# Optimization experiments

Hardware: AMD Instinct MI355X
Metric: run time of the kernel (lower is better)

## Reference

```python
import jax, jax.numpy as jnp
import numpy as np

B, A, V, D = 16, 1024, 1024, 512


def setup_inputs() -> dict:
    key = jax.random.key(0)
    k1, k2 = jax.random.split(key)
    audio_encoded = jax.random.normal(k1, (B, A, D), dtype=jnp.float32)
    visual_encoded = jax.random.normal(k2, (B, V, D), dtype=jnp.float32)
    return {"audio_encoded": audio_encoded, "visual_encoded": visual_encoded}


def reference(audio_encoded, visual_encoded):
    # Batched pairwise L2 distance: out[b, a, v] = ||audio[b,a] - visual[b,v]||_2
    # Fused ||a||^2 + ||v||^2 - 2 a.v formulation (single batched GEMM) replacing
    # the original per-(batch, audio-frame) Python loop of diff/pow/sum/sqrt.
    a_sq = jnp.sum(audio_encoded * audio_encoded, axis=-1)   # [B, A]
    v_sq = jnp.sum(visual_encoded * visual_encoded, axis=-1)  # [B, V]
    cross = jnp.einsum("bad,bvd->bav", audio_encoded, visual_encoded)  # [B, A, V]
    dist_sq = a_sq[:, :, None] + v_sq[:, None, :] - 2.0 * cross
    dist_sq = jnp.maximum(dist_sq, 0.0)  # clamp fp round-off negatives
    l2_features = jnp.sqrt(dist_sq)  # [B, A, V]
    return l2_features
```

## Files before the change

### kernel.cpp

```cpp
#include <hip/hip_runtime.h>
#include <hip/hip_bf16.h>

typedef __attribute__((ext_vector_type(8))) short short8;
typedef __attribute__((ext_vector_type(4))) float fv4;

constexpr int B_ = 16, A_ = 1024, V_ = 1024, D_ = 512;

__device__ __forceinline__ unsigned cvtpk(float lo, float hi) {
    unsigned r;
    asm("v_cvt_pk_bf16_f32 %0, %1, %2" : "=v"(r) : "v"(lo), "v"(hi));
    return r;
}
#define SB0() __builtin_amdgcn_sched_barrier(0)

struct Stage { fv4 x0, x1, x2, x3; };

__global__ void __launch_bounds__(512, 2)
l2dist_fused256(const float* __restrict__ audio, const float* __restrict__ visual,
                float* __restrict__ out)
{
    __shared__ __align__(16) char sA[2 * 256 * 128];
    __shared__ __align__(16) char sB[2 * 256 * 128];
    __shared__ float lnrm[512];

    const int t = threadIdx.x, lane = t & 63, w = t >> 6;
    const int wm = w >> 2, wn = w & 3;

    const int orig = blockIdx.x;
    const int wg   = (orig & 7) * 32 + (orig >> 3);
    const int b = wg >> 4, tile = wg & 15, ab = tile >> 2, vb = tile & 3;

    const float* Ag = audio  + ((size_t)b * A_ + ab * 256) * D_;
    const float* Vg = visual + ((size_t)b * V_ + vb * 256) * D_;

    const int rg  = t >> 2;
    const int lq  = t & 3;
    const int key = rg & 7;

    const float* g0 = Ag + (size_t)rg * D_ + lq * 4;
    const float* g1 = Ag + (size_t)(128 + rg) * D_ + lq * 4;
    const float* g2 = Vg + (size_t)rg * D_ + lq * 4;
    const float* g3 = Vg + (size_t)(128 + rg) * D_ + lq * 4;

    const int oLo = rg * 128;
    const int oHi = (128 + rg) * 128;

    float ps0 = 0.f, ps1 = 0.f, ps2 = 0.f, ps3 = 0.f;

#define ISSUE(S, gbase, koff) do {                                   \
        const float* _p = (gbase) + (koff);                          \
        S.x0 = *(const fv4*)(_p);      S.x1 = *(const fv4*)(_p + 16);\
        S.x2 = *(const fv4*)(_p + 32); S.x3 = *(const fv4*)(_p + 48);\
    } while (0)

#define PROC(S, dst, rowoff, ps) do {                                            \
        ps += S.x0[0]*S.x0[0] + S.x0[1]*S.x0[1] + S.x0[2]*S.x0[2] + S.x0[3]*S.x0[3] \
            + S.x1[0]*S.x1[0] + S.x1[1]*S.x1[1] + S.x1[2]*S.x1[2] + S.x1[3]*S.x1[3] \
            + S.x2[0]*S.x2[0] + S.x2[1]*S.x2[1] + S.x2[2]*S.x2[2] + S.x2[3]*S.x2[3] \
            + S.x3[0]*S.x3[0] + S.x3[1]*S.x3[1] + S.x3[2]*S.x3[2] + S.x3[3]*S.x3[3];\
        char* _d = (dst) + (rowoff);                                             \
        { int2 _v; _v.x = (int)cvtpk(S.x0[0], S.x0[1]); _v.y = (int)cvtpk(S.x0[2], S.x0[3]); \
          *(int2*)(_d + ((((0 + (lq >> 1)) ^ key) << 4) + (lq & 1) * 8)) = _v; } \
        { int2 _v; _v.x = (int)cvtpk(S.x1[0], S.x1[1]); _v.y = (int)cvtpk(S.x1[2], S.x1[3]); \
          *(int2*)(_d + ((((2 + (lq >> 1)) ^ key) << 4) + (lq & 1) * 8)) = _v; } \
        { int2 _v; _v.x = (int)cvtpk(S.x2[0], S.x2[1]); _v.y = (int)cvtpk(S.x2[2], S.x2[3]); \
          *(int2*)(_d + ((((4 + (lq >> 1)) ^ key) << 4) + (lq & 1) * 8)) = _v; } \
        { int2 _v; _v.x = (int)cvtpk(S.x3[0], S.x3[1]); _v.y = (int)cvtpk(S.x3[2], S.x3[3]); \
          *(int2*)(_d + ((((6 + (lq >> 1)) ^ key) << 4) + (lq & 1) * 8)) = _v; } \
    } while (0)

    Stage q0, q1, q2, q3;
    {
        Stage p0, p1, p2, p3;
        ISSUE(p0, g0, 0); ISSUE(p1, g1, 0); ISSUE(p2, g2, 0); ISSUE(p3, g3, 0); SB0();
        PROC(p0, sA, oLo, ps0);
        PROC(p1, sA, oHi, ps1);
        PROC(p2, sB, oLo, ps2);
        PROC(p3, sB, oHi, ps3);
    }
    ISSUE(q0, g0, 64); ISSUE(q1, g1, 64); SB0();
    __syncthreads();

    fv4 acc[8][4];
#pragma unroll
    for (int m = 0; m < 8; ++m)
#pragma unroll
        for (int n = 0; n < 4; ++n) acc[m][n] = fv4{0.f, 0.f, 0.f, 0.f};

    const int frow = lane & 15, fg = lane >> 4, xk = frow & 7;
    const int cof0 = ((0 + fg) ^ xk) << 4;
    const int cof1 = ((4 + fg) ^ xk) << 4;

#pragma unroll 1
    for (int kt = 0; kt < 8; ++kt) {
        const int cur = kt & 1;
        char* dstA = sA + (cur ^ 1) * 32768;
        char* dstB = sB + (cur ^ 1) * 32768;
        const char* Ab = sA + cur * 32768 + (wm * 128 + frow) * 128;
        const char* Bb = sB + cur * 32768 + (wn * 64 + frow) * 128;
        const int koff = (kt + 1) * 64;
        const bool st = (kt < 7);

        short8 av[4][2];
        {
            short8 bv[2][2];
#pragma unroll
            for (int m = 0; m < 4; ++m) {
                av[m][0] = *(const short8*)(Ab + m * 2048 + cof0);
                av[m][1] = *(const short8*)(Ab + m * 2048 + cof1);
            }
#pragma unroll
            for (int n = 0; n < 2; ++n) {
                bv[n][0] = *(const short8*)(Bb + n * 2048 + cof0);
                bv[n][1] = *(const short8*)(Bb + n * 2048 + cof1);
            }
            __builtin_amdgcn_s_setprio(1);
#pragma unroll
            for (int k = 0; k < 2; ++k)
#pragma unroll
                for (int m = 0; m < 4; ++m)
#pragma unroll
                    for (int n = 0; n < 2; ++n)
                        acc[m][n] = __builtin_amdgcn_mfma_f32_16x16x32_bf16(av[m][k], bv[n][k], acc[m][n], 0, 0, 0);
            __builtin_amdgcn_s_setprio(0);
        }
        if (st) { PROC(q0, dstA, oLo, ps0); ISSUE(q2, g2, koff); SB0(); }

        short8 bv2[2][2];
        {
#pragma unroll
            for (int n = 0; n < 2; ++n) {
                bv2[n][0] = *(const short8*)(Bb + (n + 2) * 2048 + cof0);
                bv2[n][1] = *(const short8*)(Bb + (n + 2) * 2048 + cof1);
            }
            __builtin_amdgcn_s_setprio(1);
#pragma unroll
            for (int k = 0; k < 2; ++k)
#pragma unroll
                for (int m = 0; m < 4; ++m)
#pragma unroll
                    for (int n = 0; n < 2; ++n)
                        acc[m][n + 2] = __builtin_amdgcn_mfma_f32_16x16x32_bf16(av[m][k], bv2[n][k], acc[m][n + 2], 0, 0, 0);
            __builtin_amdgcn_s_setprio(0);
        }
        if (st) { PROC(q1, dstA, oHi, ps1); ISSUE(q3, g3, koff); SB0(); }

        {
#pragma unroll
            for (int m = 0; m < 4; ++m) {
                av[m][0] = *(const short8*)(Ab + (m + 4) * 2048 + cof0);
                av[m][1] = *(const short8*)(Ab + (m + 4) * 2048 + cof1);
            }
            __builtin_amdgcn_s_setprio(1);
#pragma unroll
            for (int k = 0; k < 2; ++k)
#pragma unroll
                for (int m = 0; m < 4; ++m)
#pragma unroll
                    for (int n = 0; n < 2; ++n)
                        acc[m + 4][n + 2] = __builtin_amdgcn_mfma_f32_16x16x32_bf16(av[m][k], bv2[n][k], acc[m + 4][n + 2], 0, 0, 0);
            __builtin_amdgcn_s_setprio(0);
        }
        if (st) PROC(q2, dstB, oLo, ps2);

        {
            short8 bv[2][2];
#pragma unroll
            for (int n = 0; n < 2; ++n) {
                bv[n][0] = *(const short8*)(Bb + n * 2048 + cof0);
                bv[n][1] = *(const short8*)(Bb + n * 2048 + cof1);
            }
            __builtin_amdgcn_s_setprio(1);
#pragma unroll
            for (int k = 0; k < 2; ++k)
#pragma unroll
                for (int m = 0; m < 4; ++m)
#pragma unroll
                    for (int n = 0; n < 2; ++n)
                        acc[m + 4][n] = __builtin_amdgcn_mfma_f32_16x16x32_bf16(av[m][k], bv[n][k], acc[m + 4][n], 0, 0, 0);
            __builtin_amdgcn_s_setprio(0);
        }
        if (st) PROC(q3, dstB, oHi, ps3);

        if (kt < 6) {
            const int koff2 = (kt + 2) * 64;
            ISSUE(q0, g0, koff2); ISSUE(q1, g1, koff2); SB0();
        }

        __syncthreads();
    }

    ps0 += __shfl_xor(ps0, 1, 64); ps0 += __shfl_xor(ps0, 2, 64);
    ps1 += __shfl_xor(ps1, 1, 64); ps1 += __shfl_xor(ps1, 2, 64);
    ps2 += __shfl_xor(ps2, 1, 64); ps2 += __shfl_xor(ps2, 2, 64);
    ps3 += __shfl_xor(ps3, 1, 64); ps3 += __shfl_xor(ps3, 2, 64);
    if (lq == 0) {
        lnrm[rg]       = ps0;
        lnrm[128 + rg] = ps1;
        lnrm[256 + rg] = ps2;
        lnrm[384 + rg] = ps3;
    }
    __syncthreads();

    float* Ob = out + (size_t)b * A_ * V_ + (size_t)(ab * 256) * V_ + vb * 256;
#pragma unroll
    for (int m = 0; m < 8; ++m) {
#pragma unroll
        for (int n = 0; n < 4; ++n) {
            const int col = wn * 64 + n * 16 + frow;
            const float vsq = lnrm[256 + col];
#pragma unroll
            for (int j = 0; j < 4; ++j) {
                const int row = wm * 128 + m * 16 + fg * 4 + j;
                float d2 = lnrm[row] + vsq - 2.f * acc[m][n][j];
                Ob[(size_t)row * V_ + col] = sqrtf(fmaxf(d2, 0.f));
            }
        }
    }
#undef ISSUE
#undef PROC
}

extern "C" void kernel_launch(void* const* d_in, const int* in_sizes, int n_in,
                              void* d_out, int out_size, void* d_ws, size_t ws_size,
                              hipStream_t stream) {
    const float* audio  = (const float*)d_in[0];
    const float* visual = (const float*)d_in[1];
    float* out = (float*)d_out;
    l2dist_fused256<<<256, 512, 0, stream>>>(audio, visual, out);
}
```

Baseline: 49.17 us.

## Shrink output tiles to 128x128 with 256-thread blocks and explicit LDS reads

```diff
diff --git a/kernel.cpp b/kernel.cpp
--- a/kernel.cpp
+++ b/kernel.cpp
@@ -11,39 +11,49 @@
     asm("v_cvt_pk_bf16_f32 %0, %1, %2" : "=v"(r) : "v"(lo), "v"(hi));
     return r;
 }
-#define SB0() __builtin_amdgcn_sched_barrier(0)
+__device__ __forceinline__ unsigned lds_addr(const void* p) {
+    return (unsigned)(unsigned long long)(__attribute__((address_space(3))) const char*)p;
+}
+__device__ __forceinline__ short8 dsr128(unsigned a) {
+    short8 r;
+    asm volatile("ds_read_b128 %0, %1" : "=v"(r) : "v"(a));
+    return r;
+}
+#define SB0()  __builtin_amdgcn_sched_barrier(0)
+#define LGK0() asm volatile("s_waitcnt lgkmcnt(0)")
+#define BARX() do { SB0(); LGK0(); __builtin_amdgcn_s_barrier(); SB0(); } while (0)
 
 struct Stage { fv4 x0, x1, x2, x3; };
 
-__global__ void __launch_bounds__(512, 2)
-l2dist_fused256(const float* __restrict__ audio, const float* __restrict__ visual,
+__global__ void __launch_bounds__(256, 2)
+l2dist_fused128(const float* __restrict__ audio, const float* __restrict__ visual,
                 float* __restrict__ out)
 {
-    __shared__ __align__(16) char sA[2 * 256 * 128];
-    __shared__ __align__(16) char sB[2 * 256 * 128];
-    __shared__ float lnrm[512];
+    __shared__ __align__(16) char sA[2][128 * 128];
+    __shared__ __align__(16) char sB[2][128 * 128];
+    __shared__ float lnrm[256];
 
     const int t = threadIdx.x, lane = t & 63, w = t >> 6;
-    const int wm = w >> 2, wn = w & 3;
+    const int wm = w >> 1, wn = w & 1;
 
     const int orig = blockIdx.x;
-    const int wg   = (orig & 7) * 32 + (orig >> 3);
-    const int b = wg >> 4, tile = wg & 15, ab = tile >> 2, vb = tile & 3;
-
-    const float* Ag = audio  + ((size_t)b * A_ + ab * 256) * D_;
-    const float* Vg = visual + ((size_t)b * V_ + vb * 256) * D_;
+    const int wg   = (orig & 7) * 128 + (orig >> 3);
+    const int b = wg >> 6, tile = wg & 63, ab = tile >> 3, vb = tile & 7;
+
+    const float* Ag = audio  + ((size_t)b * A_ + ab * 128) * D_;
+    const float* Vg = visual + ((size_t)b * V_ + vb * 128) * D_;
 
     const int rg  = t >> 2;
     const int lq  = t & 3;
     const int key = rg & 7;
 
     const float* g0 = Ag + (size_t)rg * D_ + lq * 4;
-    const float* g1 = Ag + (size_t)(128 + rg) * D_ + lq * 4;
+    const float* g1 = Ag + (size_t)(64 + rg) * D_ + lq * 4;
     const float* g2 = Vg + (size_t)rg * D_ + lq * 4;
-    const float* g3 = Vg + (size_t)(128 + rg) * D_ + lq * 4;
+    const float* g3 = Vg + (size_t)(64 + rg) * D_ + lq * 4;
 
     const int oLo = rg * 128;
-    const int oHi = (128 + rg) * 128;
+    const int oHi = (64 + rg) * 128;
 
     float ps0 = 0.f, ps1 = 0.f, ps2 = 0.f, ps3 = 0.f;
 
@@ -69,51 +79,58 @@
           *(int2*)(_d + ((((6 + (lq >> 1)) ^ key) << 4) + (lq & 1) * 8)) = _v; } \
     } while (0)
 
-    Stage q0, q1, q2, q3;
     {
         Stage p0, p1, p2, p3;
         ISSUE(p0, g0, 0); ISSUE(p1, g1, 0); ISSUE(p2, g2, 0); ISSUE(p3, g3, 0); SB0();
-        PROC(p0, sA, oLo, ps0);
-        PROC(p1, sA, oHi, ps1);
-        PROC(p2, sB, oLo, ps2);
-        PROC(p3, sB, oHi, ps3);
-    }
-    ISSUE(q0, g0, 64); ISSUE(q1, g1, 64); SB0();
+        PROC(p0, (char*)sA[0], oLo, ps0);
+        PROC(p1, (char*)sA[0], oHi, ps1);
+        PROC(p2, (char*)sB[0], oLo, ps2);
+        PROC(p3, (char*)sB[0], oHi, ps3);
+    }
     __syncthreads();
 
-    fv4 acc[8][4];
-#pragma unroll
-    for (int m = 0; m < 8; ++m)
+    fv4 acc[4][4];
+#pragma unroll
+    for (int m = 0; m < 4; ++m)
 #pragma unroll
         for (int n = 0; n < 4; ++n) acc[m][n] = fv4{0.f, 0.f, 0.f, 0.f};
 
     const int frow = lane & 15, fg = lane >> 4, xk = frow & 7;
-    const int cof0 = ((0 + fg) ^ xk) << 4;
-    const int cof1 = ((4 + fg) ^ xk) << 4;
+    const unsigned cof0 = (unsigned)(((0 + fg) ^ xk) << 4);
+    const unsigned cof1 = (unsigned)(((4 + fg) ^ xk) << 4);
+    const unsigned baseA = lds_addr(&sA[0][0]);
+    const unsigned baseB = lds_addr(&sB[0][0]);
+    const unsigned arow = (unsigned)((wm * 64 + frow) * 128);
+    const unsigned brow = (unsigned)((wn * 64 + frow) * 128);
 
 #pragma unroll 1
     for (int kt = 0; kt < 8; ++kt) {
         const int cur = kt & 1;
-        char* dstA = sA + (cur ^ 1) * 32768;
-        char* dstB = sB + (cur ^ 1) * 32768;
-        const char* Ab = sA + cur * 32768 + (wm * 128 + frow) * 128;
-        const char* Bb = sB + cur * 32768 + (wn * 64 + frow) * 128;
+        char* dA = (char*)sA[cur ^ 1];
+        char* dB = (char*)sB[cur ^ 1];
+        const unsigned Ab = baseA + (unsigned)cur * 16384u + arow;
+        const unsigned Bb = baseB + (unsigned)cur * 16384u + brow;
         const int koff = (kt + 1) * 64;
         const bool st = (kt < 7);
+
+        Stage q0, q1, q2, q3;
+        if (st) { ISSUE(q0, g0, koff); ISSUE(q1, g1, koff);
+                  ISSUE(q2, g2, koff); ISSUE(q3, g3, koff); SB0(); }
 
         short8 av[4][2];
         {
             short8 bv[2][2];
 #pragma unroll
             for (int m = 0; m < 4; ++m) {
-                av[m][0] = *(const short8*)(Ab + m * 2048 + cof0);
-                av[m][1] = *(const short8*)(Ab + m * 2048 + cof1);
+                av[m][0] = dsr128(Ab + m * 2048 + cof0);
+                av[m][1] = dsr128(Ab + m * 2048 + cof1);
             }
 #pragma unroll
             for (int n = 0; n < 2; ++n) {
-                bv[n][0] = *(const short8*)(Bb + n * 2048 + cof0);
-                bv[n][1] = *(const short8*)(Bb + n * 2048 + cof1);
-            }
+                bv[n][0] = dsr128(Bb + n * 2048 + cof0);
+                bv[n][1] = dsr128(Bb + n * 2048 + cof1);
+            }
+            LGK0(); SB0();
             __builtin_amdgcn_s_setprio(1);
 #pragma unroll
             for (int k = 0; k < 2; ++k)
@@ -124,15 +141,16 @@
                         acc[m][n] = __builtin_amdgcn_mfma_f32_16x16x32_bf16(av[m][k], bv[n][k], acc[m][n], 0, 0, 0);
             __builtin_amdgcn_s_setprio(0);
         }
-        if (st) { PROC(q0, dstA, oLo, ps0); ISSUE(q2, g2, koff); SB0(); }
-
-        short8 bv2[2][2];
+        if (st) { PROC(q0, dA, oLo, ps0); PROC(q1, dA, oHi, ps1); }
+
         {
+            short8 bv[2][2];
 #pragma unroll
             for (int n = 0; n < 2; ++n) {
-                bv2[n][0] = *(const short8*)(Bb + (n + 2) * 2048 + cof0);
-                bv2[n][1] = *(const short8*)(Bb + (n + 2) * 2048 + cof1);
-            }
+                bv[n][0] = dsr128(Bb + (n + 2) * 2048 + cof0);
+                bv[n][1] = dsr128(Bb + (n + 2) * 2048 + cof1);
+            }
+            LGK0(); SB0();
             __builtin_amdgcn_s_setprio(1);
 #pragma unroll
             for (int k = 0; k < 2; ++k)
@@ -140,54 +158,12 @@
                 for (int m = 0; m < 4; ++m)
 #pragma unroll
                     for (int n = 0; n < 2; ++n)
-                        acc[m][n + 2] = __builtin_amdgcn_mfma_f32_16x16x32_bf16(av[m][k], bv2[n][k], acc[m][n + 2], 0, 0, 0);
+                        acc[m][n + 2] = __builtin_amdgcn_mfma_f32_16x16x32_bf16(av[m][k], bv[n][k], acc[m][n + 2], 0, 0, 0);
             __builtin_amdgcn_s_setprio(0);
         }
-        if (st) { PROC(q1, dstA, oHi, ps1); ISSUE(q3, g3, koff); SB0(); }
-
-        {
-#pragma unroll
-            for (int m = 0; m < 4; ++m) {
-                av[m][0] = *(const short8*)(Ab + (m + 4) * 2048 + cof0);
-                av[m][1] = *(const short8*)(Ab + (m + 4) * 2048 + cof1);
-            }
-            __builtin_amdgcn_s_setprio(1);
-#pragma unroll
-            for (int k = 0; k < 2; ++k)
-#pragma unroll
-                for (int m = 0; m < 4; ++m)
-#pragma unroll
-                    for (int n = 0; n < 2; ++n)
-                        acc[m + 4][n + 2] = __builtin_amdgcn_mfma_f32_16x16x32_bf16(av[m][k], bv2[n][k], acc[m + 4][n + 2], 0, 0, 0);
-            __builtin_amdgcn_s_setprio(0);
-        }
-        if (st) PROC(q2, dstB, oLo, ps2);
-
-        {
-            short8 bv[2][2];
-#pragma unroll
-            for (int n = 0; n < 2; ++n) {
-                bv[n][0] = *(const short8*)(Bb + n * 2048 + cof0);
-                bv[n][1] = *(const short8*)(Bb + n * 2048 + cof1);
-            }
-            __builtin_amdgcn_s_setprio(1);
-#pragma unroll
-            for (int k = 0; k < 2; ++k)
-#pragma unroll
-                for (int m = 0; m < 4; ++m)
-#pragma unroll
-                    for (int n = 0; n < 2; ++n)
-                        acc[m + 4][n] = __builtin_amdgcn_mfma_f32_16x16x32_bf16(av[m][k], bv[n][k], acc[m + 4][n], 0, 0, 0);
-            __builtin_amdgcn_s_setprio(0);
-        }
-        if (st) PROC(q3, dstB, oHi, ps3);
-
-        if (kt < 6) {
-            const int koff2 = (kt + 2) * 64;
-            ISSUE(q0, g0, koff2); ISSUE(q1, g1, koff2); SB0();
-        }
-
-        __syncthreads();
+        if (st) { PROC(q2, dB, oLo, ps2); PROC(q3, dB, oHi, ps3); }
+
+        BARX();
     }
 
     ps0 += __shfl_xor(ps0, 1, 64); ps0 += __shfl_xor(ps0, 2, 64);
@@ -196,22 +172,22 @@
     ps3 += __shfl_xor(ps3, 1, 64); ps3 += __shfl_xor(ps3, 2, 64);
     if (lq == 0) {
         lnrm[rg]       = ps0;
-        lnrm[128 + rg] = ps1;
-        lnrm[256 + rg] = ps2;
-        lnrm[384 + rg] = ps3;
+        lnrm[64 + rg]  = ps1;
+        lnrm[128 + rg] = ps2;
+        lnrm[192 + rg] = ps3;
     }
     __syncthreads();
 
-    float* Ob = out + (size_t)b * A_ * V_ + (size_t)(ab * 256) * V_ + vb * 256;
-#pragma unroll
-    for (int m = 0; m < 8; ++m) {
+    float* Ob = out + (size_t)b * A_ * V_ + (size_t)(ab * 128) * V_ + vb * 128;
+#pragma unroll
+    for (int m = 0; m < 4; ++m) {
 #pragma unroll
         for (int n = 0; n < 4; ++n) {
             const int col = wn * 64 + n * 16 + frow;
-            const float vsq = lnrm[256 + col];
+            const float vsq = lnrm[128 + col];
 #pragma unroll
             for (int j = 0; j < 4; ++j) {
-                const int row = wm * 128 + m * 16 + fg * 4 + j;
+                const int row = wm * 64 + m * 16 + fg * 4 + j;
                 float d2 = lnrm[row] + vsq - 2.f * acc[m][n][j];
                 Ob[(size_t)row * V_ + col] = sqrtf(fmaxf(d2, 0.f));
             }
@@ -227,5 +203,5 @@
     const float* audio  = (const float*)d_in[0];
     const float* visual = (const float*)d_in[1];
     float* out = (float*)d_out;
-    l2dist_fused256<<<256, 512, 0, stream>>>(audio, visual, out);
-}
+    l2dist_fused128<<<1024, 256, 0, stream>>>(audio, visual, out);
+}
```

Result: no change. 48.45 us (-1.5%).
